# Optimization experiments

Hardware: AMD Instinct MI355X
Metric: run time of the kernel (lower is better)

Reference implementation:

```python
import jax, jax.numpy as jnp
import numpy as np

T, D_IN, D_INT, D_OUT, B = 4096, 256, 256, 256, 8


def setup_inputs() -> dict:
    key = jax.random.key(0)
    ks = jax.random.split(key, 12)
    s_in = 1.0 / np.sqrt(D_IN)
    s_int = 1.0 / np.sqrt(D_INT)
    return {
        "x_batched": jax.random.normal(ks[0], (B, 1, T, D_IN), dtype=jnp.float32),
        "d_gamma_batched": jax.random.uniform(ks[1], (T, T), dtype=jnp.float32),
        "Wq": jax.random.uniform(ks[2], (D_IN, D_INT), jnp.float32, -s_in, s_in),
        "bq": jax.random.uniform(ks[3], (D_INT,), jnp.float32, -s_in, s_in),
        "Wk": jax.random.uniform(ks[4], (D_IN, D_INT), jnp.float32, -s_in, s_in),
        "bk": jax.random.uniform(ks[5], (D_INT,), jnp.float32, -s_in, s_in),
        "Wv": jax.random.uniform(ks[6], (D_IN, D_INT), jnp.float32, -s_in, s_in),
        "bv": jax.random.uniform(ks[7], (D_INT,), jnp.float32, -s_in, s_in),
        "Wo": jax.random.uniform(ks[8], (D_INT, D_OUT), jnp.float32, -s_int, s_int),
        "bo": jax.random.uniform(ks[9], (D_OUT,), jnp.float32, -s_int, s_int),
        "prelu_a": jnp.float32(0.25),  # PReLU single shared parameter, torch default init
    }


def reference(x_batched, d_gamma_batched, Wq, bq, Wk, bk, Wv, bv, Wo, bo, prelu_a):
    # x_batched: [B, 1, T, D_in] -> per-sample [T, D_in]
    x = x_batched.reshape(x_batched.shape[0], T, D_IN)  # [B, T, D_in]
    q = x @ Wq + bq  # [B, T, D_int]
    k = x @ Wk + bk
    v = x @ Wv + bv
    scores = jnp.einsum('btd,bsd->bts', q, k)  # [B, T, T] QK^T per sample
    retained = jnp.einsum('bts,bsd->btd', d_gamma_batched * scores, v)  # decay-gated, matmul V
    y = retained @ Wo + bo  # [B, T, D_out]
    out = jnp.where(y >= 0, y, prelu_a * y)  # PReLU
    return out  # [B, num_nodes=T, D_out]
```

## Files before the change

kernel.cpp:

```cpp
#include <hip/hip_runtime.h>

typedef unsigned short u16;
typedef __bf16 bf16x8 __attribute__((ext_vector_type(8)));
typedef float f32x4 __attribute__((ext_vector_type(4)));
typedef u16 u16x8 __attribute__((ext_vector_type(8)));

constexpr int T_DIM = 4096;
constexpr int DH    = 256;

__device__ __forceinline__ u16 f2bf(float f) {
    union { float f; unsigned u; } v; v.f = f;
    return (u16)((v.u + 0x7FFFu + ((v.u >> 16) & 1u)) >> 16);
}

__device__ __forceinline__ void gload_lds(const void* g, void* l) {
    __builtin_amdgcn_global_load_lds(
        (const __attribute__((address_space(1))) void*)g,
        (__attribute__((address_space(3))) void*)l, 16, 0, 0);
}

__global__ __launch_bounds__(256) void prep_w(
    const float* __restrict__ Wq, const float* __restrict__ Wk,
    const float* __restrict__ Wv, const float* __restrict__ Wo,
    u16* __restrict__ Wqt, u16* __restrict__ Wkt,
    u16* __restrict__ Wvt, u16* __restrict__ Wot)
{
    int idx = blockIdx.x * 256 + threadIdx.x;
    int j = idx >> 8, k = idx & 255;
    int s = k * 256 + j;
    Wqt[idx] = f2bf(Wq[s]);
    Wkt[idx] = f2bf(Wk[s]);
    Wvt[idx] = f2bf(Wv[s]);
    Wot[idx] = f2bf(Wo[s]);
}

__global__ __launch_bounds__(512, 2) void qkv_kernel(
    const float* __restrict__ x,
    const u16* __restrict__ Wqt, const u16* __restrict__ Wkt, const u16* __restrict__ Wvt,
    const float* __restrict__ bq, const float* __restrict__ bk, const float* __restrict__ bv,
    u16* __restrict__ Qg, u16* __restrict__ Kg, u16* __restrict__ Vtg)
{
    __shared__ __align__(16) char lds[131072];
    char* xl = lds;
    const int tid = threadIdx.x;
    const int w = tid >> 6, l = tid & 63;
    const int lr = l & 15, lh = l >> 4;
    const long row0 = (long)blockIdx.x * 128;
    const long bb   = row0 >> 12;
    const int  t0   = (int)(row0 & 4095);

    const u16*  Wt3[3] = { Wqt, Wkt, Wvt };
    const float* b3[3] = { bq, bk, bv };

    {
        char* wb = lds + 65536;
        const char* ws = (const char*)Wqt;
        #pragma unroll
        for (int i = 0; i < 4; ++i) {
            int off = tid * 16 + i * 8192;
            int roww = off >> 9, slot = (off >> 4) & 31;
            gload_lds(ws + roww * 512 + ((slot * 16) ^ ((roww & 7) << 4)), wb + off);
        }
    }
    #pragma unroll
    for (int i = 0; i < 8; ++i) {
        int sid = tid + i * 512;
        int row = sid >> 5, slot = sid & 31;
        const float* src = x + (row0 + row) * DH + slot * 8;
        float4 a  = *(const float4*)(src);
        float4 b2 = *(const float4*)(src + 4);
        u16x8 p;
        p[0] = f2bf(a.x);  p[1] = f2bf(a.y);  p[2] = f2bf(a.z);  p[3] = f2bf(a.w);
        p[4] = f2bf(b2.x); p[5] = f2bf(b2.y); p[6] = f2bf(b2.z); p[7] = f2bf(b2.w);
        *(u16x8*)(xl + row * 512 + ((slot * 16) ^ ((row & 7) << 4))) = p;
    }
    __syncthreads();

    bf16x8 af[8];
    const int arow = w * 16 + lr;
    #pragma unroll
    for (int ks = 0; ks < 8; ++ks)
        af[ks] = *(const bf16x8*)(xl + arow * 512 + ((ks * 64 + lh * 16) ^ ((arow & 7) << 4)));

    for (int p = 0; p < 12; ++p) {
        char* wb = lds + 65536 + (p & 1) * 32768;
        if (p < 11) {
            int pn = p + 1;
            const char* ws = (const char*)Wt3[pn >> 2] + (pn & 3) * 32768;
            char* wn = lds + 65536 + (pn & 1) * 32768;
            #pragma unroll
            for (int i = 0; i < 4; ++i) {
                int off = tid * 16 + i * 8192;
                int roww = off >> 9, slot = (off >> 4) & 31;
                gload_lds(ws + roww * 512 + ((slot * 16) ^ ((roww & 7) << 4)), wn + off);
            }
        }
        const int tgt = p >> 2, qtr = p & 3;
        f32x4 acc[4] = {};
        #pragma unroll
        for (int ks = 0; ks < 8; ++ks) {
            #pragma unroll
            for (int n = 0; n < 4; ++n) {
                int nl = n * 16 + lr;
                bf16x8 bf = *(const bf16x8*)(wb + nl * 512 + ((ks * 64 + lh * 16) ^ ((nl & 7) << 4)));
                acc[n] = __builtin_amdgcn_mfma_f32_16x16x32_bf16(af[ks], bf, acc[n], 0, 0, 0);
            }
        }
        const float* bias = b3[tgt];
        if (tgt < 2) {
            u16* dst = (tgt == 0) ? Qg : Kg;
            long grow = row0 + w * 16 + lh * 4;
            #pragma unroll
            for (int n = 0; n < 4; ++n) {
                int col = qtr * 64 + n * 16 + lr;
                float bbv = bias[col];
                #pragma unroll
                for (int r = 0; r < 4; ++r)
                    dst[(grow + r) * DH + col] = f2bf(acc[n][r] + bbv);
            }
        } else {
            #pragma unroll
            for (int n = 0; n < 4; ++n) {
                int d = qtr * 64 + n * 16 + lr;
                float bbv = bias[d];
                #pragma unroll
                for (int r = 0; r < 4; ++r) {
                    int t = w * 16 + lh * 4 + r;
                    *(u16*)(xl + d * 256 + ((t * 2) ^ ((d & 7) << 4))) = f2bf(acc[n][r] + bbv);
                }
            }
        }
        __syncthreads();
    }

    #pragma unroll
    for (int i = 0; i < 8; ++i) {
        int sid = tid + i * 512;
        int d = sid >> 4, slot = sid & 15;
        u16x8 v = *(const u16x8*)(xl + d * 256 + ((slot * 16) ^ ((d & 7) << 4)));
        *(u16x8*)((char*)Vtg + ((bb * DH + d) * T_DIM + t0) * 2 + slot * 16) = v;
    }
}

__global__ __launch_bounds__(512, 2) void retention_kernel(
    const u16* __restrict__ Qg, const u16* __restrict__ Kg, const u16* __restrict__ Vtg,
    const float* __restrict__ gamma, const u16* __restrict__ Wot,
    const float* __restrict__ bo, const float* __restrict__ pa,
    float* __restrict__ out)
{
    __shared__ __align__(16) char base[147456];
    char* pl = base + 131072;
    const int tid = threadIdx.x;
    const int w = tid >> 6, l = tid & 63;
    const int lr = l & 15, lh = l >> 4;
    const int wq = w >> 1, dh = w & 1;
    const int b  = blockIdx.x >> 5;
    const int q0 = (blockIdx.x & 31) * 128;

    const char* kgb = (const char*)(Kg + (long)b * T_DIM * DH);
    const char* vgb = (const char*)Vtg + (long)b * DH * T_DIM * 2;
    const float* gwave = gamma + (long)(q0 + wq * 32) * T_DIM + dh * 32;

    bf16x8 qf[2][8];
    #pragma unroll
    for (int rg = 0; rg < 2; ++rg) {
        const char* qb = (const char*)(Qg + ((long)b * T_DIM + q0 + wq * 32 + rg * 16 + lr) * DH);
        #pragma unroll
        for (int ks = 0; ks < 8; ++ks)
            qf[rg][ks] = *(const bf16x8*)(qb + ks * 64 + lh * 16);
    }

    f32x4 acc[2][8] = {};

    {
        char* kn = base;
        #pragma unroll
        for (int i = 0; i < 4; ++i) {
            int off = w * 4096 + i * 1024 + l * 16;
            int row = off >> 9, slot = (off >> 4) & 31;
            gload_lds(kgb + row * 512 + ((slot * 16) ^ ((row & 7) << 4)),
                      kn + w * 4096 + i * 1024);
        }
        char* vn = base + 32768;
        #pragma unroll
        for (int i = 0; i < 4; ++i) {
            int off = w * 4096 + i * 1024 + l * 16;
            int row = off >> 7, slot = (off >> 4) & 7;
            gload_lds(vgb + (long)row * (T_DIM * 2) + ((slot * 16) ^ ((row & 7) << 4)),
                      vn + w * 4096 + i * 1024);
        }
    }
    __syncthreads();

    for (int it = 0; it < 64; ++it) {
        const int s0 = it * 64;
        char* kl = base + (it & 1) * 65536;
        char* vl = kl + 32768;

        float gv0[2][4], gv1[2][4];
        {
            const float* gp = gwave + s0;
            #pragma unroll
            for (int n = 0; n < 2; ++n)
                #pragma unroll
                for (int r = 0; r < 4; ++r) {
                    gv0[n][r] = gp[(long)(lh * 4 + r) * T_DIM + n * 16 + lr];
                    gv1[n][r] = gp[(long)(16 + lh * 4 + r) * T_DIM + n * 16 + lr];
                }
        }
        __builtin_amdgcn_sched_barrier(0);

        if (it < 63) {
            const char* kg = kgb + (long)(s0 + 64) * 512;
            char* kn = base + ((it + 1) & 1) * 65536;
            #pragma unroll
            for (int i = 0; i < 4; ++i) {
                int off = w * 4096 + i * 1024 + l * 16;
                int row = off >> 9, slot = (off >> 4) & 31;
                gload_lds(kg + row * 512 + ((slot * 16) ^ ((row & 7) << 4)),
                          kn + w * 4096 + i * 1024);
            }
            const char* vg = vgb + (long)(s0 + 64) * 2;
            char* vn = kn + 32768;
            #pragma unroll
            for (int i = 0; i < 4; ++i) {
                int off = w * 4096 + i * 1024 + l * 16;
                int row = off >> 7, slot = (off >> 4) & 7;
                gload_lds(vg + (long)row * (T_DIM * 2) + ((slot * 16) ^ ((row & 7) << 4)),
                          vn + w * 4096 + i * 1024);
            }
        }

        #pragma unroll
        for (int n = 0; n < 2; ++n) {
            f32x4 sa = {}, sb = {};
            const int srow = dh * 32 + n * 16 + lr;
            #pragma unroll
            for (int ks = 0; ks < 8; ++ks) {
                bf16x8 kf = *(const bf16x8*)(kl + srow * 512 + ((ks * 64 + lh * 16) ^ ((srow & 7) << 4)));
                sa = __builtin_amdgcn_mfma_f32_16x16x32_bf16(qf[0][ks], kf, sa, 0, 0, 0);
                sb = __builtin_amdgcn_mfma_f32_16x16x32_bf16(qf[1][ks], kf, sb, 0, 0, 0);
            }
            const int cb = (dh * 32 + n * 16 + lr) * 2;
            #pragma unroll
            for (int r = 0; r < 4; ++r) {
                int pr0 = wq * 32 + lh * 4 + r;
                int pr1 = pr0 + 16;
                *(u16*)(pl + pr0 * 128 + (cb ^ ((pr0 & 7) << 4))) = f2bf(gv0[n][r] * sa[r]);
                *(u16*)(pl + pr1 * 128 + (cb ^ ((pr1 & 7) << 4))) = f2bf(gv1[n][r] * sb[r]);
            }
        }

        __builtin_amdgcn_sched_barrier(0);
        asm volatile("s_waitcnt lgkmcnt(0)" ::: "memory");
        __builtin_amdgcn_s_barrier();
        __builtin_amdgcn_sched_barrier(0);

        bf16x8 pa2[2][2];
        #pragma unroll
        for (int rg = 0; rg < 2; ++rg)
            #pragma unroll
            for (int k2 = 0; k2 < 2; ++k2) {
                int prr = wq * 32 + rg * 16 + lr;
                pa2[rg][k2] = *(const bf16x8*)(pl + prr * 128 + ((k2 * 64 + lh * 16) ^ ((prr & 7) << 4)));
            }
        #pragma unroll
        for (int n = 0; n < 8; ++n) {
            int vrow = dh * 128 + n * 16 + lr;
            #pragma unroll
            for (int k2 = 0; k2 < 2; ++k2) {
                bf16x8 bv = *(const bf16x8*)(vl + vrow * 128 + ((k2 * 64 + lh * 16) ^ ((vrow & 7) << 4)));
                acc[0][n] = __builtin_amdgcn_mfma_f32_16x16x32_bf16(pa2[0][k2], bv, acc[0][n], 0, 0, 0);
                acc[1][n] = __builtin_amdgcn_mfma_f32_16x16x32_bf16(pa2[1][k2], bv, acc[1][n], 0, 0, 0);
            }
        }
        __syncthreads();
    }

    {
        #pragma unroll
        for (int rg = 0; rg < 2; ++rg)
            #pragma unroll
            for (int n = 0; n < 8; ++n) {
                int d2 = (dh * 128 + n * 16 + lr) * 2;
                #pragma unroll
                for (int r = 0; r < 4; ++r) {
                    int q = wq * 32 + rg * 16 + lh * 4 + r;
                    *(u16*)(base + q * 512 + (d2 ^ ((q & 7) << 4))) = f2bf(acc[rg][n][r]);
                }
            }
    }
    __syncthreads();
    {
        const int arow = w * 16 + lr;
        f32x4 acc2[16] = {};
        #pragma unroll
        for (int ks = 0; ks < 8; ++ks) {
            bf16x8 a = *(const bf16x8*)(base + arow * 512 +
                        ((ks * 64 + lh * 16) ^ ((arow & 7) << 4)));
            #pragma unroll
            for (int n = 0; n < 16; ++n) {
                bf16x8 bf = *(const bf16x8*)(Wot + (n * 16 + lr) * DH + ks * 32 + lh * 8);
                acc2[n] = __builtin_amdgcn_mfma_f32_16x16x32_bf16(a, bf, acc2[n], 0, 0, 0);
            }
        }
        const float alpha = pa[0];
        long grow = (long)b * T_DIM + q0 + w * 16 + lh * 4;
        #pragma unroll
        for (int n = 0; n < 16; ++n) {
            int col = n * 16 + lr;
            float bb = bo[col];
            #pragma unroll
            for (int r = 0; r < 4; ++r) {
                float y = acc2[n][r] + bb;
                out[(grow + r) * DH + col] = (y >= 0.f) ? y : alpha * y;
            }
        }
    }
}

extern "C" void kernel_launch(void* const* d_in, const int* in_sizes, int n_in,
                              void* d_out, int out_size, void* d_ws, size_t ws_size,
                              hipStream_t stream)
{
    const float* x     = (const float*)d_in[0];
    const float* gamma = (const float*)d_in[1];
    const float* Wq = (const float*)d_in[2];
    const float* bq = (const float*)d_in[3];
    const float* Wk = (const float*)d_in[4];
    const float* bk = (const float*)d_in[5];
    const float* Wv = (const float*)d_in[6];
    const float* bv = (const float*)d_in[7];
    const float* Wo = (const float*)d_in[8];
    const float* bo = (const float*)d_in[9];
    const float* pa = (const float*)d_in[10];
    float* out = (float*)d_out;

    char* ws = (char*)d_ws;
    const long SZ = 16777216L;
    u16* Wqt = (u16*)(ws);
    u16* Wkt = (u16*)(ws + 131072);
    u16* Wvt = (u16*)(ws + 262144);
    u16* Wot = (u16*)(ws + 393216);
    u16* Qg  = (u16*)(ws + 524288);
    u16* Kg  = (u16*)(ws + 524288 + SZ);
    u16* Vtg = (u16*)(ws + 524288 + 2 * SZ);

    hipLaunchKernelGGL(prep_w, dim3(256), dim3(256), 0, stream,
                       Wq, Wk, Wv, Wo, Wqt, Wkt, Wvt, Wot);
    hipLaunchKernelGGL(qkv_kernel, dim3(256), dim3(512), 0, stream,
                       x, Wqt, Wkt, Wvt, bq, bk, bv, Qg, Kg, Vtg);
    hipLaunchKernelGGL(retention_kernel, dim3(256), dim3(512), 0, stream,
                       Qg, Kg, Vtg, gamma, Wot, bo, pa, out);
}
```

Measured before the change: 226.0 us.

## Give each wave a private score tile to drop the mid-iteration block barrier

Each wave now computes the full 32x64 gated score tile for its query rows and stores it in a per-wave LDS region, instead of splitting the tile across two waves that share a buffer. This removes the block-wide barrier between the QK^T stage and the PV stage. In exchange, QK^T MFMA work and gamma loads per wave double, and LDS usage grows to 160KB, which may reduce blocks per CU.

```diff
diff --git a/kernel.cpp b/kernel.cpp
--- a/kernel.cpp
+++ b/kernel.cpp
@@ -148,8 +148,7 @@
     const float* __restrict__ bo, const float* __restrict__ pa,
     float* __restrict__ out)
 {
-    __shared__ __align__(16) char base[147456];
-    char* pl = base + 131072;
+    __shared__ __align__(16) char base[163840];
     const int tid = threadIdx.x;
     const int w = tid >> 6, l = tid & 63;
     const int lr = l & 15, lh = l >> 4;
@@ -157,9 +156,10 @@
     const int b  = blockIdx.x >> 5;
     const int q0 = (blockIdx.x & 31) * 128;
 
+    char* pb = base + 131072 + w * 4096;
     const char* kgb = (const char*)(Kg + (long)b * T_DIM * DH);
     const char* vgb = (const char*)Vtg + (long)b * DH * T_DIM * 2;
-    const float* gwave = gamma + (long)(q0 + wq * 32) * T_DIM + dh * 32;
+    const float* gwave = gamma + (long)(q0 + wq * 32) * T_DIM;
 
     bf16x8 qf[2][8];
     #pragma unroll
@@ -197,16 +197,16 @@
         char* kl = base + (it & 1) * 65536;
         char* vl = kl + 32768;
 
-        float gv0[2][4], gv1[2][4];
+        float gv[2][4][4];
         {
             const float* gp = gwave + s0;
             #pragma unroll
-            for (int n = 0; n < 2; ++n)
+            for (int rg = 0; rg < 2; ++rg)
                 #pragma unroll
-                for (int r = 0; r < 4; ++r) {
-                    gv0[n][r] = gp[(long)(lh * 4 + r) * T_DIM + n * 16 + lr];
-                    gv1[n][r] = gp[(long)(16 + lh * 4 + r) * T_DIM + n * 16 + lr];
-                }
+                for (int n = 0; n < 4; ++n)
+                    #pragma unroll
+                    for (int r = 0; r < 4; ++r)
+                        gv[rg][n][r] = gp[(long)(rg * 16 + lh * 4 + r) * T_DIM + n * 16 + lr];
         }
         __builtin_amdgcn_sched_barrier(0);
 
@@ -232,37 +232,32 @@
         }
 
         #pragma unroll
-        for (int n = 0; n < 2; ++n) {
+        for (int n = 0; n < 4; ++n) {
             f32x4 sa = {}, sb = {};
-            const int srow = dh * 32 + n * 16 + lr;
+            const int srow = n * 16 + lr;
             #pragma unroll
             for (int ks = 0; ks < 8; ++ks) {
                 bf16x8 kf = *(const bf16x8*)(kl + srow * 512 + ((ks * 64 + lh * 16) ^ ((srow & 7) << 4)));
                 sa = __builtin_amdgcn_mfma_f32_16x16x32_bf16(qf[0][ks], kf, sa, 0, 0, 0);
                 sb = __builtin_amdgcn_mfma_f32_16x16x32_bf16(qf[1][ks], kf, sb, 0, 0, 0);
             }
-            const int cb = (dh * 32 + n * 16 + lr) * 2;
+            const int cb = (n * 16 + lr) * 2;
             #pragma unroll
             for (int r = 0; r < 4; ++r) {
-                int pr0 = wq * 32 + lh * 4 + r;
+                int pr0 = lh * 4 + r;
                 int pr1 = pr0 + 16;
-                *(u16*)(pl + pr0 * 128 + (cb ^ ((pr0 & 7) << 4))) = f2bf(gv0[n][r] * sa[r]);
-                *(u16*)(pl + pr1 * 128 + (cb ^ ((pr1 & 7) << 4))) = f2bf(gv1[n][r] * sb[r]);
-            }
-        }
-
-        __builtin_amdgcn_sched_barrier(0);
-        asm volatile("s_waitcnt lgkmcnt(0)" ::: "memory");
-        __builtin_amdgcn_s_barrier();
-        __builtin_amdgcn_sched_barrier(0);
+                *(u16*)(pb + pr0 * 128 + (cb ^ ((pr0 & 7) << 4))) = f2bf(gv[0][n][r] * sa[r]);
+                *(u16*)(pb + pr1 * 128 + (cb ^ ((pr1 & 7) << 4))) = f2bf(gv[1][n][r] * sb[r]);
+            }
+        }
 
         bf16x8 pa2[2][2];
         #pragma unroll
         for (int rg = 0; rg < 2; ++rg)
             #pragma unroll
             for (int k2 = 0; k2 < 2; ++k2) {
-                int prr = wq * 32 + rg * 16 + lr;
-                pa2[rg][k2] = *(const bf16x8*)(pl + prr * 128 + ((k2 * 64 + lh * 16) ^ ((prr & 7) << 4)));
+                int prr = rg * 16 + lr;
+                pa2[rg][k2] = *(const bf16x8*)(pb + prr * 128 + ((k2 * 64 + lh * 16) ^ ((prr & 7) << 4)));
             }
         #pragma unroll
         for (int n = 0; n < 8; ++n) {
```

Result: slower. 303.3 us (+34.2%).
